# Kernel tuning notes

Measured on AMD Instinct MI355X. Metric: run time of the kernel, lower is better.

The kernel has to match this reference:

```python
import jax, jax.numpy as jnp
import numpy as np
from jax import lax

B, T_MEL, M = 4, 63, 80
HOP, K_UP, WIN = 256, 800, 1024
R, S, Q = 120, 240, 256
NB, K, CYCLE = 16, 2, 8
PAD_UP = (K_UP + 4 * HOP - WIN) // 2  # 400
L = (T_MEL - 1) * HOP  # 15872


def conv1d(x, w, b, dilation=1, pad=(0, 0)):
    # x: [B,Cin,L], w: [Cout,Cin,K]
    y = lax.conv_general_dilated(x, w, (1,), [pad], rhs_dilation=(dilation,),
                                 dimension_numbers=('NCH', 'OIH', 'NCH'))
    return y + b[None, :, None]


def setup_inputs() -> dict:
    key = jax.random.key(0)
    ks = jax.random.split(key, 20)
    rn = lambda k, shape, s=0.05: (jax.random.normal(k, shape, jnp.float32) * s)
    return {
        'waveforms': jax.random.normal(ks[0], (B, L), jnp.float32),
        'melspecs': jax.random.normal(ks[1], (B, M, T_MEL), jnp.float32),
        # ConvTranspose1d weight, torch layout (in, out, k)
        'w_up': rn(ks[2], (M, M, K_UP)), 'b_up': rn(ks[3], (M,)),
        'w_in': rn(ks[4], (R, 1, 1)), 'b_in': rn(ks[5], (R,)),
        # per-block params stacked on leading axis
        'w_gate': rn(ks[6], (NB, 2 * R, R, K)), 'b_gate': rn(ks[7], (NB, 2 * R)),
        'w_cond': rn(ks[8], (NB, 2 * R, M, 1)), 'b_cond': rn(ks[9], (NB, 2 * R)),
        'w_res': rn(ks[10], (NB, R, R, 1)), 'b_res': rn(ks[11], (NB, R)),
        'w_skip': rn(ks[12], (NB, S, R, 1)), 'b_skip': rn(ks[13], (NB, S)),
        'w_h1': rn(ks[14], (Q, S, 1)), 'b_h1': rn(ks[15], (Q,)),
        'w_h2': rn(ks[16], (Q, Q, 1)), 'b_h2': rn(ks[17], (Q,)),
    }


def reference(waveforms, melspecs, w_up, b_up, w_in, b_in, w_gate, b_gate,
              w_cond, b_cond, w_res, b_res, w_skip, b_skip, w_h1, b_h1, w_h2, b_h2):
    # upsample = ConvTranspose1d: lhs-dilated conv with flipped, transposed kernel
    wt = jnp.flip(jnp.transpose(w_up, (1, 0, 2)), -1)  # [out,in,k]
    p = K_UP - 1 - PAD_UP  # 399
    conditions = lax.conv_general_dilated(
        melspecs, wt, (1,), [(p, p)], lhs_dilation=(HOP,),
        dimension_numbers=('NCH', 'OIH', 'NCH')) + b_up[None, :, None]

    length = min(waveforms.shape[-1], conditions.shape[-1])
    wav = waveforms[..., :length]
    cond = conditions[..., :length]

    residuals = conv1d(wav[:, None, :], w_in, b_in)  # [B,R,L]
    skips = jnp.zeros((wav.shape[0], S, length), residuals.dtype)
    for i in range(NB):
        d = 2 ** (i % CYCLE)
        gated = conv1d(residuals, w_gate[i], b_gate[i], dilation=d, pad=((K - 1) * d, 0))
        gated = gated + conv1d(cond, w_cond[i], b_cond[i])
        f, g = jnp.split(gated, 2, axis=1)
        z = jnp.tanh(f) * jax.nn.sigmoid(g)  # [B,R,L]
        skips = skips + conv1d(z, w_skip[i], b_skip[i])
        residuals = residuals + conv1d(z, w_res[i], b_res[i])

    h = conv1d(jax.nn.relu(skips), w_h1, b_h1)
    logits = conv1d(jax.nn.relu(h), w_h2, b_h2)  # [B,Q,L]
    return logits
```

## Files before the change

### kernel.cpp

```cpp
#include <hip/hip_runtime.h>
#include <math.h>

#define B_   4
#define M_   80
#define TMEL 63
#define R_   120
#define S_   240
#define Q_   256
#define NB_  16
#define L_   15872

typedef float  f32x4  __attribute__((ext_vector_type(4)));
typedef short  bf16x8 __attribute__((ext_vector_type(8)));
typedef short  short4_t __attribute__((ext_vector_type(4)));

__device__ __forceinline__ short f2bf(float x) {
  unsigned u = __builtin_bit_cast(unsigned, x);
  u += 0x7fffu + ((u >> 16) & 1u);
  return (short)(u >> 16);
}
__device__ __forceinline__ float bf2f(unsigned short s) {
  unsigned u = ((unsigned)s) << 16;
  return __builtin_bit_cast(float, u);
}

__global__ __launch_bounds__(256) void prep_melT_kernel(
    const float* __restrict__ mel, short* __restrict__ melT)
{
  const int idx = blockIdx.x * 256 + threadIdx.x;
  if (idx >= B_ * TMEL * M_) return;
  const int m = idx % M_;
  const int i = (idx / M_) % TMEL;
  const int b = idx / (M_ * TMEL);
  melT[idx] = f2bf(mel[b * (M_ * TMEL) + m * TMEL + i]);
}

__global__ __launch_bounds__(256) void prep_wup_kernel(
    const float* __restrict__ w_up, short* __restrict__ Wup)
{
  __shared__ float T[M_][65];
  const int c  = blockIdx.x >> 4;
  const int j  = (blockIdx.x >> 2) & 3;
  const int fb = blockIdx.x & 3;
  for (int idx = threadIdx.x; idx < M_ * 64; idx += 256) {
    const int pl = idx & 63, m = idx >> 6;
    const int phi = fb * 64 + pl;
    const int dmin = (phi < 112) ? -1 : -2;
    const int dmax = (phi < 144) ? 1 : 0;
    const int delta = dmin + j;
    float v = 0.0f;
    if (delta <= dmax)
      v = w_up[m * (M_ * 800) + c * 800 + (400 + phi + 256 * delta)];
    T[m][pl] = v;
  }
  __syncthreads();
  for (int idx = threadIdx.x; idx < 64 * M_; idx += 256) {
    const int m = idx % M_, pl = idx / M_;
    const int phi = fb * 64 + pl;
    Wup[((size_t)phi * M_ + c) * 320 + j * 80 + m] = f2bf(T[m][pl]);
  }
}

#define KPU 328

__global__ __launch_bounds__(256, 2) void upsample_mfma_kernel(
    const short* __restrict__ melT, const short* __restrict__ Wup,
    const float* __restrict__ b_up, short* __restrict__ condb)
{
  __shared__ __align__(16) short Xu[64 * KPU];
  const int tid = threadIdx.x;
  const int phi = blockIdx.x;
  const int r0 = blockIdx.y * 64;
  const int dmin = (phi < 112) ? -1 : -2;

  for (int idx = tid; idx < 2560; idx += 256) {
    const int v = idx % 10;
    const int j = (idx / 10) & 3;
    const int rl = idx / 40;
    const int rho = r0 + rl;
    const int b = rho / 62;
    const int n = rho - b * 62;
    const int i = n - (dmin + j);
    int4 val = make_int4(0, 0, 0, 0);
    if (b < B_ && i >= 0 && i < TMEL)
      val = *(const int4*)&melT[((size_t)b * TMEL + i) * M_ + v * 8];
    *(int4*)&Xu[rl * KPU + j * 80 + v * 8] = val;
  }
  __syncthreads();

  const int lane = tid & 63;
  const int wv = tid >> 6;
  const int col = lane & 15;
  const int quad = lane >> 4;
  const int kq = quad * 8;

  f32x4 acc[5];
#pragma unroll
  for (int i = 0; i < 5; ++i) acc[i] = (f32x4)(0.f);
#pragma unroll
  for (int ks = 0; ks < 10; ++ks) {
    bf16x8 a = *(const bf16x8*)&Xu[(wv * 16 + col) * KPU + ks * 32 + kq];
#pragma unroll
    for (int ct = 0; ct < 5; ++ct) {
      bf16x8 b = *(const bf16x8*)(Wup + ((size_t)phi * M_ + ct * 16 + col) * 320 + ks * 32 + kq);
      acc[ct] = __builtin_amdgcn_mfma_f32_16x16x32_bf16(a, b, acc[ct], 0, 0, 0);
    }
  }
#pragma unroll
  for (int ct = 0; ct < 5; ++ct) {
    const int c = ct * 16 + col;
    const float bc = b_up[c];
#pragma unroll
    for (int reg = 0; reg < 4; ++reg) {
      const int rho = r0 + wv * 16 + quad * 4 + reg;
      if (rho < 248) {
        const int b = rho / 62;
        const int n = rho - b * 62;
        const int t = phi + (n << 8);
        condb[((size_t)b * L_ + t) * M_ + c] = f2bf(acc[ct][reg] + bc);
      }
    }
  }
}

__global__ __launch_bounds__(256) void in_conv_kernel(
    const float* __restrict__ wav, const float* __restrict__ w_in,
    const float* __restrict__ b_in, short* __restrict__ res)
{
  const int idx = blockIdx.x * 256 + threadIdx.x;
  const int r = idx & 127;
  const int rem = idx >> 7;
  const int t = rem % L_;
  const int b = rem / L_;
  res[idx] = (r < R_) ? f2bf(w_in[r] * wav[b * L_ + t] + b_in[r]) : (short)0;
}

__global__ __launch_bounds__(256) void prepack_w1_kernel(
    const float* __restrict__ wg, const float* __restrict__ wc,
    short* __restrict__ W1p)
{
  const int idx = blockIdx.x * 256 + threadIdx.x;
  const int k = idx % 320;
  const int cp = (idx / 320) % 256;
  const int i = idx / (320 * 256);
  int corig = -1;
  if (cp < 128) { if (cp < 120) corig = cp; }
  else          { const int c = cp - 128; if (c < 120) corig = 120 + c; }
  float val = 0.0f;
  if (corig >= 0) {
    if (k < 120)      val = wg[((size_t)(i * 240 + corig) * 120 + k) * 2 + 0];
    else if (k < 240) val = wg[((size_t)(i * 240 + corig) * 120 + (k - 120)) * 2 + 1];
    else              val = wc[(size_t)(i * 240 + corig) * 80 + (k - 240)];
  }
  W1p[idx] = f2bf(val);
}

__global__ __launch_bounds__(256) void prepack_w2_kernel(
    const float* __restrict__ wsk, const float* __restrict__ wr,
    short* __restrict__ W2p)
{
  const int idx = blockIdx.x * 256 + threadIdx.x;
  const int k = idx % 128;
  const int sp = (idx / 128) % 384;
  const int i = idx / (128 * 384);
  float val = 0.0f;
  if (k < 120) {
    if (sp < 240)      val = wsk[(size_t)(i * 240 + sp) * 120 + k];
    else if (sp < 360) val = wr[(size_t)(i * 120 + (sp - 240)) * 120 + k];
  }
  W2p[idx] = f2bf(val);
}

__global__ __launch_bounds__(256) void prepack_rest_kernel(
    const float* __restrict__ wh1, const float* __restrict__ wh2,
    const float* __restrict__ bg, const float* __restrict__ bc,
    const float* __restrict__ bs, const float* __restrict__ br,
    short* __restrict__ Wh1p, short* __restrict__ Wh2p,
    float* __restrict__ bias1p, float* __restrict__ bias2p)
{
  const int idx = blockIdx.x * 256 + threadIdx.x;
  if (idx < 65536) {
    const int q = idx >> 8, k = idx & 255;
    Wh1p[idx] = f2bf(k < 240 ? wh1[q * 240 + k] : 0.0f);
  } else if (idx < 131072) {
    Wh2p[idx - 65536] = f2bf(wh2[idx - 65536]);
  } else if (idx < 135168) {
    const int j = idx - 131072;
    const int i = j >> 8, cp = j & 255;
    float v = 0.0f;
    if (cp < 128) { if (cp < 120) v = bg[i * 240 + cp] + bc[i * 240 + cp]; }
    else { const int c = cp - 128; if (c < 120) v = bg[i * 240 + 120 + c] + bc[i * 240 + 120 + c]; }
    bias1p[j] = v;
  } else if (idx < 141312) {
    const int j = idx - 135168;
    const int i = j / 384, sp = j % 384;
    float v = 0.0f;
    if (sp < 240)      v = bs[i * 240 + sp];
    else if (sp < 360) v = br[i * 120 + (sp - 240)];
    bias2p[j] = v;
  }
}

#define KP1 320
#define SGP 248
#define NTILE (L_ / 64)
#define NWG   (NTILE * B_)
#define CPX   (NWG / 8)

__device__ __forceinline__ int xswz(int row, int k) {
  return row * KP1 + (k ^ ((row & 7) << 3));
}

__global__ __launch_bounds__(512, 4) void block_mfma_kernel(
    const short* __restrict__ res_in, short* __restrict__ res_out,
    unsigned short* __restrict__ skips, const short* __restrict__ condb,
    const short* __restrict__ W1, const short* __restrict__ W2,
    const float* __restrict__ bias1, const float* __restrict__ bias2,
    const int d, const int first)
{
  __shared__ __align__(16) short Xs[64 * KP1];

  const int tid = threadIdx.x;
  const int w_id = blockIdx.y * NTILE + blockIdx.x;
  const int nid  = (w_id & 7) * CPX + (w_id >> 3);
  const int bb   = nid / NTILE;
  const int t0   = (nid - bb * NTILE) * 64;

  {
    const int dd = (d <= 64) ? d : 64;
    const int nr = 64 + dd;
    for (int idx = tid; idx < nr * 15; idx += 512) {
      const int rr = idx / 15, c8 = idx - rr * 15;
      int ts;
      if (d <= 64)      ts = t0 - d + rr;
      else              ts = (rr < 64) ? (t0 - 128 + rr) : (t0 + rr - 64);
      int4 v = make_int4(0, 0, 0, 0);
      if (ts >= 0)
        v = *(const int4*)(res_in + ((size_t)(bb * L_ + ts) * 128 + c8 * 8));
      if (rr < 64)
        *(int4*)&Xs[xswz(rr, c8 * 8)] = v;
      const int r1 = rr - dd;
      if (r1 >= 0)
        *(int4*)&Xs[xswz(r1, 120 + c8 * 8)] = v;
    }
  }
  for (int idx = tid; idx < 640; idx += 512) {
    const int c = idx % 10, trw = idx / 10;
    const int4 v = *(const int4*)(condb + ((size_t)(bb * L_ + t0 + trw) * M_ + c * 8));
    *(int4*)&Xs[xswz(trw, 240 + c * 8)] = v;
  }
  __syncthreads();

  const int lane = tid & 63;
  const int wv = tid >> 6;
  const int col = lane & 15;
  const int quad = lane >> 4;
  const int kq = quad * 8;

  f32x4 acc[4][2];
#pragma unroll
  for (int a = 0; a < 4; ++a)
#pragma unroll
    for (int b = 0; b < 2; ++b) acc[a][b] = (f32x4)(0.f);
  __builtin_amdgcn_s_setprio(1);
#pragma unroll
  for (int ks = 0; ks < 10; ++ks) {
    bf16x8 av[4];
#pragma unroll
    for (int tf = 0; tf < 4; ++tf)
      av[tf] = *(const bf16x8*)&Xs[xswz(tf * 16 + col, ks * 32 + kq)];
#pragma unroll
    for (int ct = 0; ct < 2; ++ct) {
      const int cpt = ((ct == 0) ? wv : (wv + 8)) * 16 + col;
      bf16x8 b = *(const bf16x8*)(W1 + cpt * 320 + ks * 32 + kq);
#pragma unroll
      for (int tf = 0; tf < 4; ++tf)
        acc[tf][ct] = __builtin_amdgcn_mfma_f32_16x16x32_bf16(av[tf], b, acc[tf][ct], 0, 0, 0);
    }
  }
  __builtin_amdgcn_s_setprio(0);

  __syncthreads();

  {
    const int ch = wv * 16 + col;
    if (ch < 120) {
      const float bf_ = bias1[ch];
      const float bg_ = bias1[128 + ch];
#pragma unroll
      for (int tf = 0; tf < 4; ++tf) {
#pragma unroll
        for (int reg = 0; reg < 4; ++reg) {
          float f = acc[tf][0][reg] + bf_;
          float g = acc[tf][1][reg] + bg_;
          f = fminf(fmaxf(f, -15.f), 15.f);
          g = fminf(fmaxf(g, -15.f), 15.f);
          const float ef = __expf(2.0f * f);
          const float th = (ef - 1.0f) * __builtin_amdgcn_rcpf(ef + 1.0f);
          const float eg = __expf(-g);
          const float sg = __builtin_amdgcn_rcpf(1.0f + eg);
          const int t = tf * 16 + quad * 4 + reg;
          Xs[xswz(t, ch)] = f2bf(th * sg);
        }
      }
    }
  }
  if (tid < 64)
    *(int4*)&Xs[xswz(tid, 240)] = make_int4(0, 0, 0, 0);
  __syncthreads();

  const size_t srow = ((size_t)bb * L_ + t0) * 240;
  int4 sk0 = make_int4(0,0,0,0), sk1 = sk0, sk2 = sk0, sk3 = sk0;
  if (!first) {
    {
      const int idx = tid;
      const int row = idx / 30, j = idx - row * 30;
      sk0 = *(const int4*)(skips + srow + row * 240 + j * 8);
    }
    {
      const int idx = tid + 512;
      const int row = idx / 30, j = idx - row * 30;
      sk1 = *(const int4*)(skips + srow + row * 240 + j * 8);
    }
    {
      const int idx = tid + 1024;
      const int row = idx / 30, j = idx - row * 30;
      sk2 = *(const int4*)(skips + srow + row * 240 + j * 8);
    }
    if (tid + 1536 < 1920) {
      const int idx = tid + 1536;
      const int row = idx / 30, j = idx - row * 30;
      sk3 = *(const int4*)(skips + srow + row * 240 + j * 8);
    }
  }

  f32x4 acc2[4][3];
#pragma unroll
  for (int a = 0; a < 4; ++a)
#pragma unroll
    for (int b = 0; b < 3; ++b) acc2[a][b] = (f32x4)(0.f);
  __builtin_amdgcn_s_setprio(1);
#pragma unroll
  for (int ks = 0; ks < 4; ++ks) {
    const int ko = ks * 32 + kq;
    const int kz = (ko >= 120) ? (ko + 120) : ko;
    bf16x8 av[4];
#pragma unroll
    for (int tf = 0; tf < 4; ++tf)
      av[tf] = *(const bf16x8*)&Xs[xswz(tf * 16 + col, kz)];
#pragma unroll
    for (int st = 0; st < 3; ++st) {
      bf16x8 b = *(const bf16x8*)(W2 + ((wv * 3 + st) * 16 + col) * 128 + ks * 32 + kq);
#pragma unroll
      for (int tf = 0; tf < 4; ++tf)
        acc2[tf][st] = __builtin_amdgcn_mfma_f32_16x16x32_bf16(av[tf], b, acc2[tf][st], 0, 0, 0);
    }
  }
  __builtin_amdgcn_s_setprio(0);

  if (wv >= 5) {
#pragma unroll
    for (int st = 0; st < 3; ++st) {
      const int tile = wv * 3 + st;
      if (tile < 23) {
        const int s = tile * 16 + col;
        const int r = s - 240;
        if (r < 120) {
          const float b2 = bias2[s];
#pragma unroll
          for (int tf = 0; tf < 4; ++tf) {
#pragma unroll
            for (int reg = 0; reg < 4; ++reg) {
              const int t = tf * 16 + quad * 4 + reg;
              const float old = bf2f((unsigned short)Xs[xswz(t, 120 + r)]);
              res_out[((size_t)(bb * L_ + t0 + t)) * 128 + r] =
                  f2bf(old + acc2[tf][st][reg] + b2);
            }
          }
        }
      }
    }
  }
  __syncthreads();

  short* SG = Xs;
  if (wv < 5) {
#pragma unroll
    for (int st = 0; st < 3; ++st) {
      const int tile = wv * 3 + st;
      const int s = tile * 16 + col;
      const float b2 = bias2[s];
#pragma unroll
      for (int tf = 0; tf < 4; ++tf)
#pragma unroll
        for (int reg = 0; reg < 4; ++reg)
          SG[(tf * 16 + quad * 4 + reg) * SGP + s] = f2bf(acc2[tf][st][reg] + b2);
    }
  }
  __syncthreads();

  {
#pragma unroll
    for (int it = 0; it < 4; ++it) {
      const int idx = tid + it * 512;
      if (idx < 1920) {
        const int row = idx / 30;
        const int j = idx - row * 30;
        unsigned short* gp = skips + srow + row * 240 + j * 8;
        int4 sv = *(const int4*)&SG[row * SGP + j * 8];
        const unsigned short* svp = (const unsigned short*)&sv;
        float vals[8];
#pragma unroll
        for (int e = 0; e < 8; ++e) vals[e] = bf2f(svp[e]);
        if (!first) {
          const int4 ov = (it == 0) ? sk0 : (it == 1) ? sk1 : (it == 2) ? sk2 : sk3;
          const unsigned short* ovp = (const unsigned short*)&ov;
#pragma unroll
          for (int e = 0; e < 8; ++e) vals[e] += bf2f(ovp[e]);
        }
        int4 res;
        unsigned short* rp = (unsigned short*)&res;
#pragma unroll
        for (int e = 0; e < 8; ++e) rp[e] = (unsigned short)f2bf(vals[e]);
        *(int4*)gp = res;
      }
    }
  }
}

#define KPH 264

__global__ __launch_bounds__(256, 2) void head_mfma_kernel(
    const unsigned short* __restrict__ skips,
    const short* __restrict__ Wh1, const short* __restrict__ Wh2,
    const float* __restrict__ bh1, const float* __restrict__ bh2,
    float* __restrict__ out)
{
  __shared__ __align__(16) short Ss[64 * KPH];
  short* const Hs = Ss;

  const int tid = threadIdx.x;
  const int w_id = blockIdx.y * NTILE + blockIdx.x;
  const int nid  = (w_id & 7) * CPX + (w_id >> 3);
  const int bb   = nid / NTILE;
  const int t0   = (nid - bb * NTILE) * 64;

  for (int idx = tid; idx < 2048; idx += 256) {
    const int c = idx & 31, trw = idx >> 5;
    if (c < 30) {
      int4 v = *(const int4*)(skips + ((size_t)(bb * L_ + t0 + trw) * 240 + c * 8));
      int* vi = (int*)&v;
#pragma unroll
      for (int j = 0; j < 4; ++j) {
        unsigned x = (unsigned)vi[j];
        unsigned lo = x & 0xFFFFu; if (lo & 0x8000u) lo = 0;
        unsigned hi = x >> 16;     if (hi & 0x8000u) hi = 0;
        vi[j] = (int)(lo | (hi << 16));
      }
      *(int4*)&Ss[trw * KPH + c * 8] = v;
    } else {
      *(int4*)&Ss[trw * KPH + c * 8] = make_int4(0, 0, 0, 0);
    }
  }
  __syncthreads();

  const int lane = tid & 63;
  const int wv = tid >> 6;
  const int col = lane & 15;
  const int quad = lane >> 4;
  const int kq = quad * 8;

  f32x4 acc[4][4];
#pragma unroll
  for (int a = 0; a < 4; ++a)
#pragma unroll
    for (int b = 0; b < 4; ++b) acc[a][b] = (f32x4)(0.f);
#pragma unroll
  for (int ks = 0; ks < 8; ++ks) {
    bf16x8 av[4];
#pragma unroll
    for (int tf = 0; tf < 4; ++tf)
      av[tf] = *(const bf16x8*)&Ss[(tf * 16 + col) * KPH + ks * 32 + kq];
#pragma unroll
    for (int ct = 0; ct < 4; ++ct) {
      bf16x8 b = *(const bf16x8*)(Wh1 + ((wv * 4 + ct) * 16 + col) * 256 + ks * 32 + kq);
#pragma unroll
      for (int tf = 0; tf < 4; ++tf)
        acc[tf][ct] = __builtin_amdgcn_mfma_f32_16x16x32_bf16(av[tf], b, acc[tf][ct], 0, 0, 0);
    }
  }

  __syncthreads();

#pragma unroll
  for (int ct = 0; ct < 4; ++ct) {
    const int q = (wv * 4 + ct) * 16 + col;
    const float b1 = bh1[q];
#pragma unroll
    for (int tf = 0; tf < 4; ++tf)
#pragma unroll
      for (int reg = 0; reg < 4; ++reg)
        Hs[(tf * 16 + quad * 4 + reg) * KPH + q] = f2bf(fmaxf(acc[tf][ct][reg] + b1, 0.0f));
  }
  __syncthreads();

  f32x4 acc2[4][4];
#pragma unroll
  for (int a = 0; a < 4; ++a)
#pragma unroll
    for (int b = 0; b < 4; ++b) acc2[a][b] = (f32x4)(0.f);
#pragma unroll
  for (int ks = 0; ks < 8; ++ks) {
    bf16x8 av[4];
#pragma unroll
    for (int tf = 0; tf < 4; ++tf)
      av[tf] = *(const bf16x8*)&Hs[(tf * 16 + col) * KPH + ks * 32 + kq];
#pragma unroll
    for (int ct = 0; ct < 4; ++ct) {
      bf16x8 b = *(const bf16x8*)(Wh2 + ((wv * 4 + ct) * 16 + col) * 256 + ks * 32 + kq);
#pragma unroll
      for (int tf = 0; tf < 4; ++tf)
        acc2[tf][ct] = __builtin_amdgcn_mfma_f32_16x16x32_bf16(av[tf], b, acc2[tf][ct], 0, 0, 0);
    }
  }
#pragma unroll
  for (int ct = 0; ct < 4; ++ct) {
    const int q = (wv * 4 + ct) * 16 + col;
    const float b2 = bh2[q];
#pragma unroll
    for (int tf = 0; tf < 4; ++tf) {
      const int tg0 = t0 + tf * 16 + quad * 4;
      float4 o = make_float4(acc2[tf][ct][0] + b2, acc2[tf][ct][1] + b2,
                             acc2[tf][ct][2] + b2, acc2[tf][ct][3] + b2);
      *(float4*)(out + ((size_t)(bb * Q_ + q)) * L_ + tg0) = o;
    }
  }
}

extern "C" void kernel_launch(void* const* d_in, const int* in_sizes, int n_in,
                              void* d_out, int out_size, void* d_ws, size_t ws_size,
                              hipStream_t stream) {
  const float* wav    = (const float*)d_in[0];
  const float* mel    = (const float*)d_in[1];
  const float* w_up   = (const float*)d_in[2];
  const float* b_up   = (const float*)d_in[3];
  const float* w_in   = (const float*)d_in[4];
  const float* b_in   = (const float*)d_in[5];
  const float* w_gate = (const float*)d_in[6];
  const float* b_gate = (const float*)d_in[7];
  const float* w_cond = (const float*)d_in[8];
  const float* b_cond = (const float*)d_in[9];
  const float* w_res  = (const float*)d_in[10];
  const float* b_res  = (const float*)d_in[11];
  const float* w_skip = (const float*)d_in[12];
  const float* b_skip = (const float*)d_in[13];
  const float* w_h1   = (const float*)d_in[14];
  const float* b_h1   = (const float*)d_in[15];
  const float* w_h2   = (const float*)d_in[16];
  const float* b_h2   = (const float*)d_in[17];
  float* out = (float*)d_out;

  char* w = (char*)d_ws;
  short* condb   = (short*)w;                 w += (size_t)B_ * L_ * M_ * 2;
  short* res0    = (short*)w;                 w += (size_t)B_ * L_ * 128 * 2;
  short* res1    = (short*)w;                 w += (size_t)B_ * L_ * 128 * 2;
  unsigned short* skips = (unsigned short*)w; w += (size_t)B_ * L_ * 240 * 2;
  short* W1p     = (short*)w;                 w += (size_t)16 * 256 * 320 * 2;
  short* W2p     = (short*)w;                 w += (size_t)16 * 384 * 128 * 2;
  short* Wh1p    = (short*)w;                 w += (size_t)256 * 256 * 2;
  short* Wh2p    = (short*)w;                 w += (size_t)256 * 256 * 2;
  float* bias1p  = (float*)w;                 w += (size_t)16 * 256 * 4;
  float* bias2p  = (float*)w;                 w += (size_t)16 * 384 * 4;
  short* melT    = (short*)w;                 w += (size_t)B_ * TMEL * M_ * 2;
  short* Wup = (short*)skips;

  prepack_w1_kernel<<<(16 * 256 * 320) / 256, 256, 0, stream>>>(w_gate, w_cond, W1p);
  prepack_w2_kernel<<<(16 * 384 * 128) / 256, 256, 0, stream>>>(w_skip, w_res, W2p);
  prepack_rest_kernel<<<141312 / 256, 256, 0, stream>>>(
      w_h1, w_h2, b_gate, b_cond, b_skip, b_res, Wh1p, Wh2p, bias1p, bias2p);
  prep_melT_kernel<<<(B_ * TMEL * M_ + 255) / 256, 256, 0, stream>>>(mel, melT);
  prep_wup_kernel<<<80 * 4 * 4, 256, 0, stream>>>(w_up, Wup);

  dim3 ugrid(256, 4);
  upsample_mfma_kernel<<<ugrid, 256, 0, stream>>>(melT, Wup, b_up, condb);
  in_conv_kernel<<<((size_t)B_ * L_ * 128) / 256, 256, 0, stream>>>(wav, w_in, b_in, res0);

  dim3 bgrid(L_ / 64, B_);
  for (int i = 0; i < NB_; ++i) {
    const int d = 1 << (i & 7);
    const short* rin  = (i & 1) ? res1 : res0;
    short*       rout = (i & 1) ? res0 : res1;
    block_mfma_kernel<<<bgrid, 512, 0, stream>>>(
        rin, rout, skips, condb,
        W1p + (size_t)i * 256 * 320, W2p + (size_t)i * 384 * 128,
        bias1p + i * 256, bias2p + i * 384,
        d, (i == 0) ? 1 : 0);
  }

  head_mfma_kernel<<<bgrid, 256, 0, stream>>>(skips, Wh1p, Wh2p, b_h1, b_h2, out);
}
```

Before: 1.016 ms.

## Process two time tiles per workgroup, prefetching the next tile during compute

```diff
diff --git a/kernel.cpp b/kernel.cpp
--- a/kernel.cpp
+++ b/kernel.cpp
@@ -206,57 +206,25 @@
 #define NTILE (L_ / 64)
 #define NWG   (NTILE * B_)
 #define CPX   (NWG / 8)
+#define NPAIR (L_ / 128)
+#define NWGB  (NPAIR * B_)
+#define CPXB  (NWGB / 8)
 
 __device__ __forceinline__ int xswz(int row, int k) {
   return row * KP1 + (k ^ ((row & 7) << 3));
 }
 
-__global__ __launch_bounds__(512, 4) void block_mfma_kernel(
+template<int PREF>
+__device__ __forceinline__ void tile_body(
+    short* __restrict__ Xs, const int tid, const int wv, const int col,
+    const int quad, const int kq, const int bb, const int t0,
+    const int d, const int dd, const int nr, const int first,
     const short* __restrict__ res_in, short* __restrict__ res_out,
     unsigned short* __restrict__ skips, const short* __restrict__ condb,
     const short* __restrict__ W1, const short* __restrict__ W2,
     const float* __restrict__ bias1, const float* __restrict__ bias2,
-    const int d, const int first)
-{
-  __shared__ __align__(16) short Xs[64 * KP1];
-
-  const int tid = threadIdx.x;
-  const int w_id = blockIdx.y * NTILE + blockIdx.x;
-  const int nid  = (w_id & 7) * CPX + (w_id >> 3);
-  const int bb   = nid / NTILE;
-  const int t0   = (nid - bb * NTILE) * 64;
-
-  {
-    const int dd = (d <= 64) ? d : 64;
-    const int nr = 64 + dd;
-    for (int idx = tid; idx < nr * 15; idx += 512) {
-      const int rr = idx / 15, c8 = idx - rr * 15;
-      int ts;
-      if (d <= 64)      ts = t0 - d + rr;
-      else              ts = (rr < 64) ? (t0 - 128 + rr) : (t0 + rr - 64);
-      int4 v = make_int4(0, 0, 0, 0);
-      if (ts >= 0)
-        v = *(const int4*)(res_in + ((size_t)(bb * L_ + ts) * 128 + c8 * 8));
-      if (rr < 64)
-        *(int4*)&Xs[xswz(rr, c8 * 8)] = v;
-      const int r1 = rr - dd;
-      if (r1 >= 0)
-        *(int4*)&Xs[xswz(r1, 120 + c8 * 8)] = v;
-    }
-  }
-  for (int idx = tid; idx < 640; idx += 512) {
-    const int c = idx % 10, trw = idx / 10;
-    const int4 v = *(const int4*)(condb + ((size_t)(bb * L_ + t0 + trw) * M_ + c * 8));
-    *(int4*)&Xs[xswz(trw, 240 + c * 8)] = v;
-  }
-  __syncthreads();
-
-  const int lane = tid & 63;
-  const int wv = tid >> 6;
-  const int col = lane & 15;
-  const int quad = lane >> 4;
-  const int kq = quad * 8;
-
+    int4* __restrict__ rv, int4* __restrict__ cv, const int t0n)
+{
   f32x4 acc[4][2];
 #pragma unroll
   for (int a = 0; a < 4; ++a)
@@ -310,27 +278,17 @@
   __syncthreads();
 
   const size_t srow = ((size_t)bb * L_ + t0) * 240;
-  int4 sk0 = make_int4(0,0,0,0), sk1 = sk0, sk2 = sk0, sk3 = sk0;
+  int4 sk[4];
+#pragma unroll
+  for (int i = 0; i < 4; ++i) sk[i] = make_int4(0, 0, 0, 0);
   if (!first) {
-    {
-      const int idx = tid;
-      const int row = idx / 30, j = idx - row * 30;
-      sk0 = *(const int4*)(skips + srow + row * 240 + j * 8);
-    }
-    {
-      const int idx = tid + 512;
-      const int row = idx / 30, j = idx - row * 30;
-      sk1 = *(const int4*)(skips + srow + row * 240 + j * 8);
-    }
-    {
-      const int idx = tid + 1024;
-      const int row = idx / 30, j = idx - row * 30;
-      sk2 = *(const int4*)(skips + srow + row * 240 + j * 8);
-    }
-    if (tid + 1536 < 1920) {
-      const int idx = tid + 1536;
-      const int row = idx / 30, j = idx - row * 30;
-      sk3 = *(const int4*)(skips + srow + row * 240 + j * 8);
+#pragma unroll
+    for (int i = 0; i < 4; ++i) {
+      const int idx = tid + i * 512;
+      if (idx < 1920) {
+        const int row = idx / 30, j = idx - row * 30;
+        sk[i] = *(const int4*)(skips + srow + row * 240 + j * 8);
+      }
     }
   }
 
@@ -357,6 +315,31 @@
     }
   }
   __builtin_amdgcn_s_setprio(0);
+
+  if (PREF) {
+#pragma unroll
+    for (int i = 0; i < 4; ++i) {
+      const int idx = tid + i * 512;
+      int4 v = make_int4(0, 0, 0, 0);
+      if (idx < nr * 15) {
+        const int rr = idx / 15, c8 = idx - rr * 15;
+        int ts;
+        if (d <= 64)      ts = t0n - d + rr;
+        else              ts = (rr < 64) ? (t0n - 128 + rr) : (t0n + rr - 64);
+        if (ts >= 0)
+          v = *(const int4*)(res_in + ((size_t)(bb * L_ + ts) * 128 + c8 * 8));
+      }
+      rv[i] = v;
+    }
+#pragma unroll
+    for (int i = 0; i < 2; ++i) {
+      const int idx = tid + i * 512;
+      if (idx < 640) {
+        const int c = idx % 10, trw = idx / 10;
+        cv[i] = *(const int4*)(condb + ((size_t)(bb * L_ + t0n + trw) * M_ + c * 8));
+      }
+    }
+  }
 
   if (wv >= 5) {
 #pragma unroll
@@ -399,33 +382,115 @@
   }
   __syncthreads();
 
-  {
-#pragma unroll
-    for (int it = 0; it < 4; ++it) {
-      const int idx = tid + it * 512;
-      if (idx < 1920) {
-        const int row = idx / 30;
-        const int j = idx - row * 30;
-        unsigned short* gp = skips + srow + row * 240 + j * 8;
-        int4 sv = *(const int4*)&SG[row * SGP + j * 8];
-        const unsigned short* svp = (const unsigned short*)&sv;
-        float vals[8];
-#pragma unroll
-        for (int e = 0; e < 8; ++e) vals[e] = bf2f(svp[e]);
-        if (!first) {
-          const int4 ov = (it == 0) ? sk0 : (it == 1) ? sk1 : (it == 2) ? sk2 : sk3;
-          const unsigned short* ovp = (const unsigned short*)&ov;
-#pragma unroll
-          for (int e = 0; e < 8; ++e) vals[e] += bf2f(ovp[e]);
-        }
-        int4 res;
-        unsigned short* rp = (unsigned short*)&res;
-#pragma unroll
-        for (int e = 0; e < 8; ++e) rp[e] = (unsigned short)f2bf(vals[e]);
-        *(int4*)gp = res;
-      }
-    }
-  }
+#pragma unroll
+  for (int it = 0; it < 4; ++it) {
+    const int idx = tid + it * 512;
+    if (idx < 1920) {
+      const int row = idx / 30;
+      const int j = idx - row * 30;
+      unsigned short* gp = skips + srow + row * 240 + j * 8;
+      int4 sv = *(const int4*)&SG[row * SGP + j * 8];
+      const unsigned short* svp = (const unsigned short*)&sv;
+      float vals[8];
+#pragma unroll
+      for (int e = 0; e < 8; ++e) vals[e] = bf2f(svp[e]);
+      if (!first) {
+        const unsigned short* ovp = (const unsigned short*)&sk[it];
+#pragma unroll
+        for (int e = 0; e < 8; ++e) vals[e] += bf2f(ovp[e]);
+      }
+      int4 res;
+      unsigned short* rp = (unsigned short*)&res;
+#pragma unroll
+      for (int e = 0; e < 8; ++e) rp[e] = (unsigned short)f2bf(vals[e]);
+      *(int4*)gp = res;
+    }
+  }
+}
+
+__global__ __launch_bounds__(512, 4) void block_mfma_kernel(
+    const short* __restrict__ res_in, short* __restrict__ res_out,
+    unsigned short* __restrict__ skips, const short* __restrict__ condb,
+    const short* __restrict__ W1, const short* __restrict__ W2,
+    const float* __restrict__ bias1, const float* __restrict__ bias2,
+    const int d, const int first)
+{
+  __shared__ __align__(16) short Xs[64 * KP1];
+
+  const int tid = threadIdx.x;
+  const int w_id = blockIdx.x;
+  const int nid  = (w_id & 7) * CPXB + (w_id >> 3);
+  const int bb   = nid / NPAIR;
+  const int tp   = nid - bb * NPAIR;
+  const int t0a  = tp * 128;
+  const int t0b  = t0a + 64;
+
+  const int dd = (d <= 64) ? d : 64;
+  const int nr = 64 + dd;
+
+  const int lane = tid & 63;
+  const int wv = tid >> 6;
+  const int col = lane & 15;
+  const int quad = lane >> 4;
+  const int kq = quad * 8;
+
+  for (int idx = tid; idx < nr * 15; idx += 512) {
+    const int rr = idx / 15, c8 = idx - rr * 15;
+    int ts;
+    if (d <= 64)      ts = t0a - d + rr;
+    else              ts = (rr < 64) ? (t0a - 128 + rr) : (t0a + rr - 64);
+    int4 v = make_int4(0, 0, 0, 0);
+    if (ts >= 0)
+      v = *(const int4*)(res_in + ((size_t)(bb * L_ + ts) * 128 + c8 * 8));
+    if (rr < 64)
+      *(int4*)&Xs[xswz(rr, c8 * 8)] = v;
+    const int r1 = rr - dd;
+    if (r1 >= 0)
+      *(int4*)&Xs[xswz(r1, 120 + c8 * 8)] = v;
+  }
+  for (int idx = tid; idx < 640; idx += 512) {
+    const int c = idx % 10, trw = idx / 10;
+    const int4 v = *(const int4*)(condb + ((size_t)(bb * L_ + t0a + trw) * M_ + c * 8));
+    *(int4*)&Xs[xswz(trw, 240 + c * 8)] = v;
+  }
+  __syncthreads();
+
+  int4 rv[4], cv[2];
+#pragma unroll
+  for (int i = 0; i < 4; ++i) rv[i] = make_int4(0, 0, 0, 0);
+#pragma unroll
+  for (int i = 0; i < 2; ++i) cv[i] = make_int4(0, 0, 0, 0);
+
+  tile_body<1>(Xs, tid, wv, col, quad, kq, bb, t0a, d, dd, nr, first,
+               res_in, res_out, skips, condb, W1, W2, bias1, bias2,
+               rv, cv, t0b);
+  __syncthreads();
+
+#pragma unroll
+  for (int i = 0; i < 4; ++i) {
+    const int idx = tid + i * 512;
+    if (idx < nr * 15) {
+      const int rr = idx / 15, c8 = idx - rr * 15;
+      if (rr < 64)
+        *(int4*)&Xs[xswz(rr, c8 * 8)] = rv[i];
+      const int r1 = rr - dd;
+      if (r1 >= 0)
+        *(int4*)&Xs[xswz(r1, 120 + c8 * 8)] = rv[i];
+    }
+  }
+#pragma unroll
+  for (int i = 0; i < 2; ++i) {
+    const int idx = tid + i * 512;
+    if (idx < 640) {
+      const int c = idx % 10, trw = idx / 10;
+      *(int4*)&Xs[xswz(trw, 240 + c * 8)] = cv[i];
+    }
+  }
+  __syncthreads();
+
+  tile_body<0>(Xs, tid, wv, col, quad, kq, bb, t0b, d, dd, nr, first,
+               res_in, res_out, skips, condb, W1, W2, bias1, bias2,
+               rv, cv, t0b);
 }
 
 #define KPH 264
@@ -585,17 +650,17 @@
   upsample_mfma_kernel<<<ugrid, 256, 0, stream>>>(melT, Wup, b_up, condb);
   in_conv_kernel<<<((size_t)B_ * L_ * 128) / 256, 256, 0, stream>>>(wav, w_in, b_in, res0);
 
-  dim3 bgrid(L_ / 64, B_);
   for (int i = 0; i < NB_; ++i) {
     const int d = 1 << (i & 7);
     const short* rin  = (i & 1) ? res1 : res0;
     short*       rout = (i & 1) ? res0 : res1;
-    block_mfma_kernel<<<bgrid, 512, 0, stream>>>(
+    block_mfma_kernel<<<NWGB, 512, 0, stream>>>(
         rin, rout, skips, condb,
         W1p + (size_t)i * 256 * 320, W2p + (size_t)i * 384 * 128,
         bias1p + i * 256, bias2p + i * 384,
         d, (i == 0) ? 1 : 0);
   }
 
+  dim3 bgrid(NTILE, B_);
   head_mfma_kernel<<<bgrid, 256, 0, stream>>>(skips, Wh1p, Wh2p, b_h1, b_h2, out);
 }
```

Measured after the change: 1.301 ms. +28.1%, slower.

## Defer skip projections to head kernel by storing per-block gated activations

Applied to the files above, without the earlier changes.

```diff
diff --git a/kernel.cpp b/kernel.cpp
--- a/kernel.cpp
+++ b/kernel.cpp
@@ -201,22 +201,35 @@
   }
 }
 
+__global__ __launch_bounds__(256) void sum_bs_kernel(
+    const float* __restrict__ bs, float* __restrict__ skipbias)
+{
+  const int s = blockIdx.x * 256 + threadIdx.x;
+  if (s < 240) {
+    float v = 0.0f;
+#pragma unroll
+    for (int i = 0; i < NB_; ++i) v += bs[i * 240 + s];
+    skipbias[s] = v;
+  }
+}
+
 #define KP1 320
 #define SGP 248
 #define NTILE (L_ / 64)
 #define NWG   (NTILE * B_)
 #define CPX   (NWG / 8)
+#define ZSTR  ((size_t)B_ * L_ * 128)
 
 __device__ __forceinline__ int xswz(int row, int k) {
   return row * KP1 + (k ^ ((row & 7) << 3));
 }
 
-__global__ __launch_bounds__(512, 4) void block_mfma_kernel(
+__global__ __launch_bounds__(512, 4) void block_mfma_z_kernel(
     const short* __restrict__ res_in, short* __restrict__ res_out,
-    unsigned short* __restrict__ skips, const short* __restrict__ condb,
+    short* __restrict__ zb, const short* __restrict__ condb,
     const short* __restrict__ W1, const short* __restrict__ W2,
     const float* __restrict__ bias1, const float* __restrict__ bias2,
-    const int d, const int first)
+    const int d)
 {
   __shared__ __align__(16) short Xs[64 * KP1];
 
@@ -279,7 +292,6 @@
     }
   }
   __builtin_amdgcn_s_setprio(0);
-
   __syncthreads();
 
   {
@@ -309,29 +321,319 @@
     *(int4*)&Xs[xswz(tid, 240)] = make_int4(0, 0, 0, 0);
   __syncthreads();
 
+  const int sp = (15 + wv) * 16 + col;
+  f32x4 acc2[4];
+#pragma unroll
+  for (int a = 0; a < 4; ++a) acc2[a] = (f32x4)(0.f);
+  __builtin_amdgcn_s_setprio(1);
+#pragma unroll
+  for (int ks = 0; ks < 4; ++ks) {
+    const int ko = ks * 32 + kq;
+    const int kz = (ko >= 120) ? (ko + 120) : ko;
+    bf16x8 b = *(const bf16x8*)(W2 + sp * 128 + ks * 32 + kq);
+#pragma unroll
+    for (int tf = 0; tf < 4; ++tf) {
+      bf16x8 av = *(const bf16x8*)&Xs[xswz(tf * 16 + col, kz)];
+      acc2[tf] = __builtin_amdgcn_mfma_f32_16x16x32_bf16(av, b, acc2[tf], 0, 0, 0);
+    }
+  }
+  __builtin_amdgcn_s_setprio(0);
+
+  {
+    const size_t zrow = ((size_t)(bb * L_ + t0)) * 128;
+#pragma unroll
+    for (int it = 0; it < 2; ++it) {
+      const int idx = tid + it * 512;
+      const int row = idx >> 4, j = idx & 15;
+      const int4 v = *(const int4*)&Xs[xswz(row, (j < 15) ? j * 8 : 240)];
+      *(int4*)&zb[zrow + (size_t)row * 128 + j * 8] = v;
+    }
+  }
+
+  {
+    const int r = wv * 16 + col;
+    if (r < 120) {
+      const float b2 = bias2[sp];
+#pragma unroll
+      for (int tf = 0; tf < 4; ++tf) {
+#pragma unroll
+        for (int reg = 0; reg < 4; ++reg) {
+          const int t = tf * 16 + quad * 4 + reg;
+          const float old = bf2f((unsigned short)Xs[xswz(t, 120 + r)]);
+          res_out[((size_t)(bb * L_ + t0 + t)) * 128 + r] =
+              f2bf(old + acc2[tf][reg] + b2);
+        }
+      }
+    }
+  }
+}
+
+#define KPH 264
+
+__global__ __launch_bounds__(256, 2) void head_mfma_z_kernel(
+    const short* __restrict__ zb, const short* __restrict__ W2,
+    const short* __restrict__ Wh1, const short* __restrict__ Wh2,
+    const float* __restrict__ skipbias, const float* __restrict__ bh1,
+    const float* __restrict__ bh2, float* __restrict__ out)
+{
+  __shared__ __align__(16) short Sh[64 * KPH];
+
+  const int tid = threadIdx.x;
+  const int w_id = blockIdx.y * NTILE + blockIdx.x;
+  const int nid  = (w_id & 7) * CPX + (w_id >> 3);
+  const int bb   = nid / NTILE;
+  const int t0   = (nid - bb * NTILE) * 64;
+
+  const int lane = tid & 63;
+  const int wv = tid >> 6;
+  const int col = lane & 15;
+  const int quad = lane >> 4;
+  const int kq = quad * 8;
+
+  const int r0 = tid >> 4, j0 = tid & 15;
+  const size_t gbase = ((size_t)(bb * L_ + t0)) * 128 + j0 * 8;
+
+  int4 zv0 = *(const int4*)&zb[gbase + (size_t)(r0     ) * 128];
+  int4 zv1 = *(const int4*)&zb[gbase + (size_t)(r0 + 16) * 128];
+  int4 zv2 = *(const int4*)&zb[gbase + (size_t)(r0 + 32) * 128];
+  int4 zv3 = *(const int4*)&zb[gbase + (size_t)(r0 + 48) * 128];
+
+  f32x4 acc[4][4];
+#pragma unroll
+  for (int a = 0; a < 4; ++a)
+#pragma unroll
+    for (int b = 0; b < 4; ++b) acc[a][b] = (f32x4)(0.f);
+
+  for (int i = 0; i < NB_; ++i) {
+    *(int4*)&Sh[(r0     ) * 136 + j0 * 8] = zv0;
+    *(int4*)&Sh[(r0 + 16) * 136 + j0 * 8] = zv1;
+    *(int4*)&Sh[(r0 + 32) * 136 + j0 * 8] = zv2;
+    *(int4*)&Sh[(r0 + 48) * 136 + j0 * 8] = zv3;
+    __syncthreads();
+    if (i < NB_ - 1) {
+      const short* zn = zb + (size_t)(i + 1) * ZSTR;
+      zv0 = *(const int4*)&zn[gbase + (size_t)(r0     ) * 128];
+      zv1 = *(const int4*)&zn[gbase + (size_t)(r0 + 16) * 128];
+      zv2 = *(const int4*)&zn[gbase + (size_t)(r0 + 32) * 128];
+      zv3 = *(const int4*)&zn[gbase + (size_t)(r0 + 48) * 128];
+    }
+    const short* Wl = W2 + (size_t)i * 384 * 128;
+    __builtin_amdgcn_s_setprio(1);
+#pragma unroll
+    for (int ks = 0; ks < 4; ++ks) {
+      bf16x8 av[4];
+#pragma unroll
+      for (int tf = 0; tf < 4; ++tf)
+        av[tf] = *(const bf16x8*)&Sh[(tf * 16 + col) * 136 + ks * 32 + kq];
+#pragma unroll
+      for (int ct = 0; ct < 4; ++ct) {
+        const int tile = wv * 4 + ct;
+        if (tile < 15) {
+          bf16x8 b = *(const bf16x8*)(Wl + (tile * 16 + col) * 128 + ks * 32 + kq);
+#pragma unroll
+          for (int tf = 0; tf < 4; ++tf)
+            acc[tf][ct] = __builtin_amdgcn_mfma_f32_16x16x32_bf16(av[tf], b, acc[tf][ct], 0, 0, 0);
+        }
+      }
+    }
+    __builtin_amdgcn_s_setprio(0);
+    __syncthreads();
+  }
+
+#pragma unroll
+  for (int ct = 0; ct < 4; ++ct) {
+    const int tile = wv * 4 + ct;
+    if (tile < 15) {
+      const int s = tile * 16 + col;
+      const float sb = skipbias[s];
+#pragma unroll
+      for (int tf = 0; tf < 4; ++tf)
+#pragma unroll
+        for (int reg = 0; reg < 4; ++reg)
+          Sh[(tf * 16 + quad * 4 + reg) * KPH + s] = f2bf(fmaxf(acc[tf][ct][reg] + sb, 0.0f));
+    }
+  }
+  if (tid < 128) {
+    const int row = tid >> 1, g = tid & 1;
+    *(int4*)&Sh[row * KPH + 240 + g * 8] = make_int4(0, 0, 0, 0);
+  }
+  __syncthreads();
+
+  f32x4 acc1[4][4];
+#pragma unroll
+  for (int a = 0; a < 4; ++a)
+#pragma unroll
+    for (int b = 0; b < 4; ++b) acc1[a][b] = (f32x4)(0.f);
+#pragma unroll
+  for (int ks = 0; ks < 8; ++ks) {
+    bf16x8 av[4];
+#pragma unroll
+    for (int tf = 0; tf < 4; ++tf)
+      av[tf] = *(const bf16x8*)&Sh[(tf * 16 + col) * KPH + ks * 32 + kq];
+#pragma unroll
+    for (int ct = 0; ct < 4; ++ct) {
+      bf16x8 b = *(const bf16x8*)(Wh1 + ((wv * 4 + ct) * 16 + col) * 256 + ks * 32 + kq);
+#pragma unroll
+      for (int tf = 0; tf < 4; ++tf)
+        acc1[tf][ct] = __builtin_amdgcn_mfma_f32_16x16x32_bf16(av[tf], b, acc1[tf][ct], 0, 0, 0);
+    }
+  }
+  __syncthreads();
+
+#pragma unroll
+  for (int ct = 0; ct < 4; ++ct) {
+    const int q = (wv * 4 + ct) * 16 + col;
+    const float b1 = bh1[q];
+#pragma unroll
+    for (int tf = 0; tf < 4; ++tf)
+#pragma unroll
+      for (int reg = 0; reg < 4; ++reg)
+        Sh[(tf * 16 + quad * 4 + reg) * KPH + q] = f2bf(fmaxf(acc1[tf][ct][reg] + b1, 0.0f));
+  }
+  __syncthreads();
+
+  f32x4 acc2[4][4];
+#pragma unroll
+  for (int a = 0; a < 4; ++a)
+#pragma unroll
+    for (int b = 0; b < 4; ++b) acc2[a][b] = (f32x4)(0.f);
+#pragma unroll
+  for (int ks = 0; ks < 8; ++ks) {
+    bf16x8 av[4];
+#pragma unroll
+    for (int tf = 0; tf < 4; ++tf)
+      av[tf] = *(const bf16x8*)&Sh[(tf * 16 + col) * KPH + ks * 32 + kq];
+#pragma unroll
+    for (int ct = 0; ct < 4; ++ct) {
+      bf16x8 b = *(const bf16x8*)(Wh2 + ((wv * 4 + ct) * 16 + col) * 256 + ks * 32 + kq);
+#pragma unroll
+      for (int tf = 0; tf < 4; ++tf)
+        acc2[tf][ct] = __builtin_amdgcn_mfma_f32_16x16x32_bf16(av[tf], b, acc2[tf][ct], 0, 0, 0);
+    }
+  }
+#pragma unroll
+  for (int ct = 0; ct < 4; ++ct) {
+    const int q = (wv * 4 + ct) * 16 + col;
+    const float b2 = bh2[q];
+#pragma unroll
+    for (int tf = 0; tf < 4; ++tf) {
+      const int tg0 = t0 + tf * 16 + quad * 4;
+      float4 o = make_float4(acc2[tf][ct][0] + b2, acc2[tf][ct][1] + b2,
+                             acc2[tf][ct][2] + b2, acc2[tf][ct][3] + b2);
+      *(float4*)(out + ((size_t)(bb * Q_ + q)) * L_ + tg0) = o;
+    }
+  }
+}
+
+__global__ __launch_bounds__(512, 4) void block_mfma_kernel(
+    const short* __restrict__ res_in, short* __restrict__ res_out,
+    unsigned short* __restrict__ skips, const short* __restrict__ condb,
+    const short* __restrict__ W1, const short* __restrict__ W2,
+    const float* __restrict__ bias1, const float* __restrict__ bias2,
+    const int d, const int first)
+{
+  __shared__ __align__(16) short Xs[64 * KP1];
+
+  const int tid = threadIdx.x;
+  const int w_id = blockIdx.y * NTILE + blockIdx.x;
+  const int nid  = (w_id & 7) * CPX + (w_id >> 3);
+  const int bb   = nid / NTILE;
+  const int t0   = (nid - bb * NTILE) * 64;
+
+  {
+    const int dd = (d <= 64) ? d : 64;
+    const int nr = 64 + dd;
+    for (int idx = tid; idx < nr * 15; idx += 512) {
+      const int rr = idx / 15, c8 = idx - rr * 15;
+      int ts;
+      if (d <= 64)      ts = t0 - d + rr;
+      else              ts = (rr < 64) ? (t0 - 128 + rr) : (t0 + rr - 64);
+      int4 v = make_int4(0, 0, 0, 0);
+      if (ts >= 0)
+        v = *(const int4*)(res_in + ((size_t)(bb * L_ + ts) * 128 + c8 * 8));
+      if (rr < 64)
+        *(int4*)&Xs[xswz(rr, c8 * 8)] = v;
+      const int r1 = rr - dd;
+      if (r1 >= 0)
+        *(int4*)&Xs[xswz(r1, 120 + c8 * 8)] = v;
+    }
+  }
+  for (int idx = tid; idx < 640; idx += 512) {
+    const int c = idx % 10, trw = idx / 10;
+    const int4 v = *(const int4*)(condb + ((size_t)(bb * L_ + t0 + trw) * M_ + c * 8));
+    *(int4*)&Xs[xswz(trw, 240 + c * 8)] = v;
+  }
+  __syncthreads();
+
+  const int lane = tid & 63;
+  const int wv = tid >> 6;
+  const int col = lane & 15;
+  const int quad = lane >> 4;
+  const int kq = quad * 8;
+
+  f32x4 acc[4][2];
+#pragma unroll
+  for (int a = 0; a < 4; ++a)
+#pragma unroll
+    for (int b = 0; b < 2; ++b) acc[a][b] = (f32x4)(0.f);
+  __builtin_amdgcn_s_setprio(1);
+#pragma unroll
+  for (int ks = 0; ks < 10; ++ks) {
+    bf16x8 av[4];
+#pragma unroll
+    for (int tf = 0; tf < 4; ++tf)
+      av[tf] = *(const bf16x8*)&Xs[xswz(tf * 16 + col, ks * 32 + kq)];
+#pragma unroll
+    for (int ct = 0; ct < 2; ++ct) {
+      const int cpt = ((ct == 0) ? wv : (wv + 8)) * 16 + col;
+      bf16x8 b = *(const bf16x8*)(W1 + cpt * 320 + ks * 32 + kq);
+#pragma unroll
+      for (int tf = 0; tf < 4; ++tf)
+        acc[tf][ct] = __builtin_amdgcn_mfma_f32_16x16x32_bf16(av[tf], b, acc[tf][ct], 0, 0, 0);
+    }
+  }
+  __builtin_amdgcn_s_setprio(0);
+  __syncthreads();
+
+  {
+    const int ch = wv * 16 + col;
+    if (ch < 120) {
+      const float bf_ = bias1[ch];
+      const float bg_ = bias1[128 + ch];
+#pragma unroll
+      for (int tf = 0; tf < 4; ++tf) {
+#pragma unroll
+        for (int reg = 0; reg < 4; ++reg) {
+          float f = acc[tf][0][reg] + bf_;
+          float g = acc[tf][1][reg] + bg_;
+          f = fminf(fmaxf(f, -15.f), 15.f);
+          g = fminf(fmaxf(g, -15.f), 15.f);
+          const float ef = __expf(2.0f * f);
+          const float th = (ef - 1.0f) * __builtin_amdgcn_rcpf(ef + 1.0f);
+          const float eg = __expf(-g);
+          const float sg = __builtin_amdgcn_rcpf(1.0f + eg);
+          const int t = tf * 16 + quad * 4 + reg;
+          Xs[xswz(t, ch)] = f2bf(th * sg);
+        }
+      }
+    }
+  }
+  if (tid < 64)
+    *(int4*)&Xs[xswz(tid, 240)] = make_int4(0, 0, 0, 0);
+  __syncthreads();
+
   const size_t srow = ((size_t)bb * L_ + t0) * 240;
   int4 sk0 = make_int4(0,0,0,0), sk1 = sk0, sk2 = sk0, sk3 = sk0;
   if (!first) {
-    {
-      const int idx = tid;
-      const int row = idx / 30, j = idx - row * 30;
-      sk0 = *(const int4*)(skips + srow + row * 240 + j * 8);
-    }
-    {
-      const int idx = tid + 512;
-      const int row = idx / 30, j = idx - row * 30;
-      sk1 = *(const int4*)(skips + srow + row * 240 + j * 8);
-    }
-    {
-      const int idx = tid + 1024;
-      const int row = idx / 30, j = idx - row * 30;
-      sk2 = *(const int4*)(skips + srow + row * 240 + j * 8);
-    }
+    { const int idx = tid;        const int row = idx / 30, j = idx - row * 30;
+      sk0 = *(const int4*)(skips + srow + row * 240 + j * 8); }
+    { const int idx = tid + 512;  const int row = idx / 30, j = idx - row * 30;
+      sk1 = *(const int4*)(skips + srow + row * 240 + j * 8); }
+    { const int idx = tid + 1024; const int row = idx / 30, j = idx - row * 30;
+      sk2 = *(const int4*)(skips + srow + row * 240 + j * 8); }
     if (tid + 1536 < 1920) {
-      const int idx = tid + 1536;
-      const int row = idx / 30, j = idx - row * 30;
-      sk3 = *(const int4*)(skips + srow + row * 240 + j * 8);
-    }
+      const int idx = tid + 1536; const int row = idx / 30, j = idx - row * 30;
+      sk3 = *(const int4*)(skips + srow + row * 240 + j * 8); }
   }
 
   f32x4 acc2[4][3];
@@ -399,36 +701,32 @@
   }
   __syncthreads();
 
-  {
-#pragma unroll
-    for (int it = 0; it < 4; ++it) {
-      const int idx = tid + it * 512;
-      if (idx < 1920) {
-        const int row = idx / 30;
-        const int j = idx - row * 30;
-        unsigned short* gp = skips + srow + row * 240 + j * 8;
-        int4 sv = *(const int4*)&SG[row * SGP + j * 8];
-        const unsigned short* svp = (const unsigned short*)&sv;
-        float vals[8];
-#pragma unroll
-        for (int e = 0; e < 8; ++e) vals[e] = bf2f(svp[e]);
-        if (!first) {
-          const int4 ov = (it == 0) ? sk0 : (it == 1) ? sk1 : (it == 2) ? sk2 : sk3;
-          const unsigned short* ovp = (const unsigned short*)&ov;
-#pragma unroll
-          for (int e = 0; e < 8; ++e) vals[e] += bf2f(ovp[e]);
-        }
-        int4 res;
-        unsigned short* rp = (unsigned short*)&res;
-#pragma unroll
-        for (int e = 0; e < 8; ++e) rp[e] = (unsigned short)f2bf(vals[e]);
-        *(int4*)gp = res;
+#pragma unroll
+  for (int it = 0; it < 4; ++it) {
+    const int idx = tid + it * 512;
+    if (idx < 1920) {
+      const int row = idx / 30;
+      const int j = idx - row * 30;
+      unsigned short* gp = skips + srow + row * 240 + j * 8;
+      int4 sv = *(const int4*)&SG[row * SGP + j * 8];
+      const unsigned short* svp = (const unsigned short*)&sv;
+      float vals[8];
+#pragma unroll
+      for (int e = 0; e < 8; ++e) vals[e] = bf2f(svp[e]);
+      if (!first) {
+        const int4 ov = (it == 0) ? sk0 : (it == 1) ? sk1 : (it == 2) ? sk2 : sk3;
+        const unsigned short* ovp = (const unsigned short*)&ov;
+#pragma unroll
+        for (int e = 0; e < 8; ++e) vals[e] += bf2f(ovp[e]);
       }
-    }
-  }
-}
-
-#define KPH 264
+      int4 res;
+      unsigned short* rp = (unsigned short*)&res;
+#pragma unroll
+      for (int e = 0; e < 8; ++e) rp[e] = (unsigned short)f2bf(vals[e]);
+      *(int4*)gp = res;
+    }
+  }
+}
 
 __global__ __launch_bounds__(256, 2) void head_mfma_kernel(
     const unsigned short* __restrict__ skips,
@@ -489,7 +787,6 @@
         acc[tf][ct] = __builtin_amdgcn_mfma_f32_16x16x32_bf16(av[tf], b, acc[tf][ct], 0, 0, 0);
     }
   }
-
   __syncthreads();
 
 #pragma unroll
@@ -560,42 +857,95 @@
   const float* b_h2   = (const float*)d_in[17];
   float* out = (float*)d_out;
 
-  char* w = (char*)d_ws;
-  short* condb   = (short*)w;                 w += (size_t)B_ * L_ * M_ * 2;
-  short* res0    = (short*)w;                 w += (size_t)B_ * L_ * 128 * 2;
-  short* res1    = (short*)w;                 w += (size_t)B_ * L_ * 128 * 2;
-  unsigned short* skips = (unsigned short*)w; w += (size_t)B_ * L_ * 240 * 2;
-  short* W1p     = (short*)w;                 w += (size_t)16 * 256 * 320 * 2;
-  short* W2p     = (short*)w;                 w += (size_t)16 * 384 * 128 * 2;
-  short* Wh1p    = (short*)w;                 w += (size_t)256 * 256 * 2;
-  short* Wh2p    = (short*)w;                 w += (size_t)256 * 256 * 2;
-  float* bias1p  = (float*)w;                 w += (size_t)16 * 256 * 4;
-  float* bias2p  = (float*)w;                 w += (size_t)16 * 384 * 4;
-  short* melT    = (short*)w;                 w += (size_t)B_ * TMEL * M_ * 2;
-  short* Wup = (short*)skips;
-
-  prepack_w1_kernel<<<(16 * 256 * 320) / 256, 256, 0, stream>>>(w_gate, w_cond, W1p);
-  prepack_w2_kernel<<<(16 * 384 * 128) / 256, 256, 0, stream>>>(w_skip, w_res, W2p);
-  prepack_rest_kernel<<<141312 / 256, 256, 0, stream>>>(
-      w_h1, w_h2, b_gate, b_cond, b_skip, b_res, Wh1p, Wh2p, bias1p, bias2p);
-  prep_melT_kernel<<<(B_ * TMEL * M_ + 255) / 256, 256, 0, stream>>>(mel, melT);
-  prep_wup_kernel<<<80 * 4 * 4, 256, 0, stream>>>(w_up, Wup);
-
-  dim3 ugrid(256, 4);
-  upsample_mfma_kernel<<<ugrid, 256, 0, stream>>>(melT, Wup, b_up, condb);
-  in_conv_kernel<<<((size_t)B_ * L_ * 128) / 256, 256, 0, stream>>>(wav, w_in, b_in, res0);
-
-  dim3 bgrid(L_ / 64, B_);
-  for (int i = 0; i < NB_; ++i) {
-    const int d = 1 << (i & 7);
-    const short* rin  = (i & 1) ? res1 : res0;
-    short*       rout = (i & 1) ? res0 : res1;
-    block_mfma_kernel<<<bgrid, 512, 0, stream>>>(
-        rin, rout, skips, condb,
-        W1p + (size_t)i * 256 * 320, W2p + (size_t)i * 384 * 128,
-        bias1p + i * 256, bias2p + i * 384,
-        d, (i == 0) ? 1 : 0);
-  }
-
-  head_mfma_kernel<<<bgrid, 256, 0, stream>>>(skips, Wh1p, Wh2p, b_h1, b_h2, out);
-}
+  const size_t SZ_condb = (size_t)B_ * L_ * M_ * 2;
+  const size_t SZ_res   = (size_t)B_ * L_ * 128 * 2;
+  const size_t SZ_zb    = ZSTR * 2;
+  const size_t SZ_W1p   = (size_t)16 * 256 * 320 * 2;
+  const size_t SZ_W2p   = (size_t)16 * 384 * 128 * 2;
+  const size_t SZ_Wh    = (size_t)256 * 256 * 2;
+  const size_t SZ_b1    = (size_t)16 * 256 * 4;
+  const size_t SZ_b2    = (size_t)16 * 384 * 4;
+  const size_t SZ_melT  = (size_t)B_ * TMEL * M_ * 2;
+  const size_t NEED_Z = SZ_condb + 2 * SZ_res + 16 * SZ_zb + SZ_W1p + SZ_W2p
+                      + 2 * SZ_Wh + SZ_b1 + SZ_b2 + 1024 + SZ_melT;
+
+  if (ws_size >= NEED_Z) {
+    char* w = (char*)d_ws;
+    short* condb   = (short*)w;  w += SZ_condb;
+    short* res0    = (short*)w;  w += SZ_res;
+    short* res1    = (short*)w;  w += SZ_res;
+    short* zb      = (short*)w;  w += 16 * SZ_zb;
+    short* W1p     = (short*)w;  w += SZ_W1p;
+    short* W2p     = (short*)w;  w += SZ_W2p;
+    short* Wh1p    = (short*)w;  w += SZ_Wh;
+    short* Wh2p    = (short*)w;  w += SZ_Wh;
+    float* bias1p  = (float*)w;  w += SZ_b1;
+    float* bias2p  = (float*)w;  w += SZ_b2;
+    float* skipbias= (float*)w;  w += 1024;
+    short* melT    = (short*)w;  w += SZ_melT;
+    short* Wup = zb;
+
+    prepack_w1_kernel<<<(16 * 256 * 320) / 256, 256, 0, stream>>>(w_gate, w_cond, W1p);
+    prepack_w2_kernel<<<(16 * 384 * 128) / 256, 256, 0, stream>>>(w_skip, w_res, W2p);
+    prepack_rest_kernel<<<141312 / 256, 256, 0, stream>>>(
+        w_h1, w_h2, b_gate, b_cond, b_skip, b_res, Wh1p, Wh2p, bias1p, bias2p);
+    sum_bs_kernel<<<1, 256, 0, stream>>>(b_skip, skipbias);
+    prep_melT_kernel<<<(B_ * TMEL * M_ + 255) / 256, 256, 0, stream>>>(mel, melT);
+    prep_wup_kernel<<<80 * 4 * 4, 256, 0, stream>>>(w_up, Wup);
+
+    dim3 ugrid(256, 4);
+    upsample_mfma_kernel<<<ugrid, 256, 0, stream>>>(melT, Wup, b_up, condb);
+    in_conv_kernel<<<((size_t)B_ * L_ * 128) / 256, 256, 0, stream>>>(wav, w_in, b_in, res0);
+
+    dim3 bgrid(NTILE, B_);
+    for (int i = 0; i < NB_; ++i) {
+      const int d = 1 << (i & 7);
+      const short* rin  = (i & 1) ? res1 : res0;
+      short*       rout = (i & 1) ? res0 : res1;
+      block_mfma_z_kernel<<<bgrid, 512, 0, stream>>>(
+          rin, rout, zb + (size_t)i * ZSTR, condb,
+          W1p + (size_t)i * 256 * 320, W2p + (size_t)i * 384 * 128,
+          bias1p + i * 256, bias2p + i * 384, d);
+    }
+    head_mfma_z_kernel<<<bgrid, 256, 0, stream>>>(
+        zb, W2p, Wh1p, Wh2p, skipbias, b_h1, b_h2, out);
+  } else {
+    char* w = (char*)d_ws;
+    short* condb   = (short*)w;                 w += SZ_condb;
+    short* res0    = (short*)w;                 w += SZ_res;
+    short* res1    = (short*)w;                 w += SZ_res;
+    unsigned short* skips = (unsigned short*)w; w += (size_t)B_ * L_ * 240 * 2;
+    short* W1p     = (short*)w;                 w += SZ_W1p;
+    short* W2p     = (short*)w;                 w += SZ_W2p;
+    short* Wh1p    = (short*)w;                 w += SZ_Wh;
+    short* Wh2p    = (short*)w;                 w += SZ_Wh;
+    float* bias1p  = (float*)w;                 w += SZ_b1;
+    float* bias2p  = (float*)w;                 w += SZ_b2;
+    short* melT    = (short*)w;                 w += SZ_melT;
+    short* Wup = (short*)skips;
+
+    prepack_w1_kernel<<<(16 * 256 * 320) / 256, 256, 0, stream>>>(w_gate, w_cond, W1p);
+    prepack_w2_kernel<<<(16 * 384 * 128) / 256, 256, 0, stream>>>(w_skip, w_res, W2p);
+    prepack_rest_kernel<<<141312 / 256, 256, 0, stream>>>(
+        w_h1, w_h2, b_gate, b_cond, b_skip, b_res, Wh1p, Wh2p, bias1p, bias2p);
+    prep_melT_kernel<<<(B_ * TMEL * M_ + 255) / 256, 256, 0, stream>>>(mel, melT);
+    prep_wup_kernel<<<80 * 4 * 4, 256, 0, stream>>>(w_up, Wup);
+
+    dim3 ugrid(256, 4);
+    upsample_mfma_kernel<<<ugrid, 256, 0, stream>>>(melT, Wup, b_up, condb);
+    in_conv_kernel<<<((size_t)B_ * L_ * 128) / 256, 256, 0, stream>>>(wav, w_in, b_in, res0);
+
+    dim3 bgrid(NTILE, B_);
+    for (int i = 0; i < NB_; ++i) {
+      const int d = 1 << (i & 7);
+      const short* rin  = (i & 1) ? res1 : res0;
+      short*       rout = (i & 1) ? res0 : res1;
+      block_mfma_kernel<<<bgrid, 512, 0, stream>>>(
+          rin, rout, skips, condb,
+          W1p + (size_t)i * 256 * 320, W2p + (size_t)i * 384 * 128,
+          bias1p + i * 256, bias2p + i * 384,
+          d, (i == 0) ? 1 : 0);
+    }
+    head_mfma_kernel<<<bgrid, 256, 0, stream>>>(skips, Wh1p, Wh2p, b_h1, b_h2, out);
+  }
+}
```

New measurement: 1.017 ms. About the same (+0.1%).
